# Performance work log

Measured on AMD Instinct MI355X. Metric: run time of the kernel, lower is better.

The kernel has to match this reference:

```python
import jax, jax.numpy as jnp
import numpy as np

B, S, D = 1, 4096, 1024
H, DK, DV = 16, 64, 64


def setup_inputs() -> dict:
    key = jax.random.key(0)
    ks = jax.random.split(key, 12)
    s = 0.02
    return {
        "queries": jax.random.normal(ks[0], (B, S, D), jnp.float32),
        "keys": jax.random.normal(ks[1], (B, S, D), jnp.float32),
        "values": jax.random.normal(ks[2], (B, S, D), jnp.float32),
        "Wq": jax.random.normal(ks[3], (H * DK, D), jnp.float32) * s,
        "bq": jnp.zeros((H * DK,), jnp.float32),
        "Wk": jax.random.normal(ks[4], (H * DK, D), jnp.float32) * s,
        "bk": jnp.zeros((H * DK,), jnp.float32),
        "Wv": jax.random.normal(ks[5], (H * DV, D), jnp.float32) * s,
        "bv": jnp.zeros((H * DV,), jnp.float32),
        "Wo": jax.random.normal(ks[6], (D, H * DV), jnp.float32) * s,
        "bo": jnp.zeros((D,), jnp.float32),
    }


def reference(queries, keys, values, Wq, bq, Wk, bk, Wv, bv, Wo, bo):
    b, sq, _ = queries.shape
    sk = keys.shape[1]
    # projections -> [b, h, s, d]
    q = (queries @ Wq.T + bq).reshape(b, sq, H, DK).transpose(0, 2, 1, 3)
    k = (keys @ Wk.T + bk).reshape(b, sk, H, DK).transpose(0, 2, 1, 3)
    v = (values @ Wv.T + bv).reshape(b, sk, H, DV).transpose(0, 2, 1, 3)
    scores = jnp.einsum('bhqd,bhkd->bhqk', q, k) / jnp.sqrt(jnp.float32(DK))
    # causal mask (is_causal=True): disallow j > i
    causal = jnp.triu(jnp.ones((sq, sk), bool), k=1)
    scores = jnp.where(causal, jnp.float32(-jnp.inf), scores)
    attn = jax.nn.softmax(scores, axis=-1)
    out = jnp.einsum('bhqk,bhkd->bhqd', attn, v)
    out = out.transpose(0, 2, 1, 3).reshape(b, sq, H * DV)
    return out @ Wo.T + bo
```

## Files before the change

### kernel.cpp

```cpp
#include <hip/hip_runtime.h>

#define DEVI __device__ __forceinline__

typedef __attribute__((ext_vector_type(8))) short bf16x8;
typedef __attribute__((ext_vector_type(4))) float f32x4;
typedef __attribute__((ext_vector_type(16))) float f32x16;

#define SQL 4096
#define DM 1024
#define NH 16
#define HD 64
#define S64 (SQL * HD)

DEVI unsigned short f2bf(float f) {
  unsigned int u = __float_as_uint(f);
  unsigned int r = (u + 0x7FFFu + ((u >> 16) & 1u)) >> 16;
  return (unsigned short)r;
}

DEVI void gl16(const void* g, void* l) {
  __builtin_amdgcn_global_load_lds((const __attribute__((address_space(1))) void*)g,
                                   (__attribute__((address_space(3))) void*)l, 16, 0, 0);
}

DEVI f32x4 mfma16(bf16x8 a, bf16x8 b, f32x4 c) {
  return __builtin_amdgcn_mfma_f32_16x16x32_bf16(a, b, c, 0, 0, 0);
}
DEVI f32x16 mfma32(bf16x8 a, bf16x8 b, f32x16 c) {
  return __builtin_amdgcn_mfma_f32_32x32x16_bf16(a, b, c, 0, 0, 0);
}

DEVI unsigned cvtpk(float lo, float hi) {
  unsigned r;
  asm("v_cvt_pk_bf16_f32 %0, %1, %2" : "=v"(r) : "v"(lo), "v"(hi));
  return r;
}

__global__ void cvt_all(const float* __restrict__ q, const float* __restrict__ k,
                        const float* __restrict__ v, const float* __restrict__ Wq,
                        const float* __restrict__ Wk, const float* __restrict__ Wv,
                        const float* __restrict__ Wo, unsigned short* __restrict__ o) {
  const size_t SD = (size_t)SQL * DM, DD = (size_t)DM * DM;
  size_t i = ((size_t)blockIdx.x * 256 + threadIdx.x) * 4;
  const float* src;
  size_t base;
  if (i < SD) { src = q; base = 0; }
  else if (i < 2 * SD) { src = k; base = SD; }
  else if (i < 3 * SD) { src = v; base = 2 * SD; }
  else if (i < 3 * SD + DD) { src = Wq; base = 3 * SD; }
  else if (i < 3 * SD + 2 * DD) { src = Wk; base = 3 * SD + DD; }
  else if (i < 3 * SD + 3 * DD) { src = Wv; base = 3 * SD + 2 * DD; }
  else { src = Wo; base = 3 * SD + 3 * DD; }
  float4 vv = *reinterpret_cast<const float4*>(src + (i - base));
  ushort4 ov;
  ov.x = f2bf(vv.x); ov.y = f2bf(vv.y); ov.z = f2bf(vv.z); ov.w = f2bf(vv.w);
  *reinterpret_cast<ushort4*>(o + i) = ov;
}

__global__ __launch_bounds__(256) void gemm_qkv(
    const unsigned short* __restrict__ xq, const unsigned short* __restrict__ xk,
    const unsigned short* __restrict__ xv, const unsigned short* __restrict__ wq,
    const unsigned short* __restrict__ wk, const unsigned short* __restrict__ wv,
    const float* __restrict__ bq, const float* __restrict__ bk, const float* __restrict__ bv,
    unsigned short* __restrict__ Qh, unsigned short* __restrict__ Kh,
    unsigned short* __restrict__ VT) {
  __shared__ __align__(16) unsigned short smem[17408];
  unsigned short* lA = smem;
  unsigned short* lB = smem + 8192;
  const int z = blockIdx.z;
  const unsigned short* A = (z == 0) ? xq : (z == 1) ? xk : xv;
  const unsigned short* B = (z == 0) ? wq : (z == 1) ? wk : wv;
  const float* bias = (z == 0) ? bq : (z == 1) ? bk : bv;

  const int t = threadIdx.x;
  const int wid = t >> 6, lane = t & 63, lr = lane & 15, lg = lane >> 4;
  const int wm = wid >> 1, wn = wid & 1;
  const int m0 = blockIdx.y * 128, n0 = blockIdx.x * 128;
  const int K = DM;

  f32x4 acc[4][4] = {};

  for (int kb = 0; kb < K; kb += 64) {
    __syncthreads();
#pragma unroll
    for (int i = 0; i < 4; i++) {
      const int u = i * 256 + t;
      const int row = u >> 3;
      const int ke = (u & 7) * 8;
      unsigned short* la = lA + (size_t)(i * 256 + wid * 64) * 8;
      unsigned short* lb = lB + (size_t)(i * 256 + wid * 64) * 8;
      gl16(A + (size_t)(m0 + row) * K + kb + ke, la);
      gl16(B + (size_t)(n0 + row) * K + kb + ke, lb);
    }
    __syncthreads();
#pragma unroll
    for (int kk = 0; kk < 2; kk++) {
      bf16x8 af[4], bfr[4];
#pragma unroll
      for (int m = 0; m < 4; m++)
        af[m] = *reinterpret_cast<const bf16x8*>(&lA[(wm * 64 + m * 16 + lr) * 64 + kk * 32 + lg * 8]);
#pragma unroll
      for (int n = 0; n < 4; n++)
        bfr[n] = *reinterpret_cast<const bf16x8*>(&lB[(wn * 64 + n * 16 + lr) * 64 + kk * 32 + lg * 8]);
#pragma unroll
      for (int m = 0; m < 4; m++)
#pragma unroll
        for (int n = 0; n < 4; n++)
          acc[m][n] = mfma16(af[m], bfr[n], acc[m][n]);
    }
  }

  if (z < 2) {
    const float sc = (z == 0) ? 0.18033688f : 1.0f;
    unsigned short* dst = (z == 0) ? Qh : Kh;
#pragma unroll
    for (int m = 0; m < 4; m++)
#pragma unroll
      for (int n = 0; n < 4; n++) {
        const int col = n0 + wn * 64 + n * 16 + lr;
        const int hh = col >> 6, d = col & 63;
        const int row0 = m0 + wm * 64 + m * 16 + lg * 4;
        const float bsv = bias[col];
#pragma unroll
        for (int r = 0; r < 4; r++)
          dst[(size_t)hh * S64 + (size_t)(row0 + r) * HD + d] = f2bf((acc[m][n][r] + bsv) * sc);
      }
  } else {
    __syncthreads();
#pragma unroll
    for (int m = 0; m < 4; m++)
#pragma unroll
      for (int n = 0; n < 4; n++) {
        const int col = n0 + wn * 64 + n * 16 + lr;
        const int dt = wn * 64 + n * 16 + lr;
        const float bsv = bias[col];
#pragma unroll
        for (int r = 0; r < 4; r++) {
          const int st = wm * 64 + m * 16 + lg * 4 + r;
          smem[dt * 136 + st] = f2bf(acc[m][n][r] + bsv);
        }
      }
    __syncthreads();
#pragma unroll
    for (int it = 0; it < 8; it++) {
      const int u = it * 256 + t;
      const int d = u >> 4, sc8 = (u & 15) * 8;
      const int col = n0 + d, hh = col >> 6, dd = col & 63;
      *reinterpret_cast<uint4*>(VT + (size_t)hh * S64 + (size_t)dd * SQL + m0 + sc8) =
          *reinterpret_cast<const uint4*>(&smem[d * 136 + sc8]);
    }
  }
}

__global__ __launch_bounds__(256) void gemm_out(
    const unsigned short* __restrict__ A, const unsigned short* __restrict__ B,
    const float* __restrict__ bias, float* __restrict__ C) {
  __shared__ __align__(16) unsigned short lA[128 * 64];
  __shared__ __align__(16) unsigned short lB[128 * 64];
  const int t = threadIdx.x;
  const int wid = t >> 6, lane = t & 63, lr = lane & 15, lg = lane >> 4;
  const int wm = wid >> 1, wn = wid & 1;
  const int m0 = blockIdx.y * 128, n0 = blockIdx.x * 128;
  const int K = DM, N = DM;

  f32x4 acc[4][4] = {};

  for (int kb = 0; kb < K; kb += 64) {
    __syncthreads();
#pragma unroll
    for (int i = 0; i < 4; i++) {
      const int u = i * 256 + t;
      const int row = u >> 3;
      const int ke = (u & 7) * 8;
      unsigned short* la = lA + (size_t)(i * 256 + wid * 64) * 8;
      unsigned short* lb = lB + (size_t)(i * 256 + wid * 64) * 8;
      gl16(A + (size_t)(m0 + row) * K + kb + ke, la);
      gl16(B + (size_t)(n0 + row) * K + kb + ke, lb);
    }
    __syncthreads();
#pragma unroll
    for (int kk = 0; kk < 2; kk++) {
      bf16x8 af[4], bfr[4];
#pragma unroll
      for (int m = 0; m < 4; m++)
        af[m] = *reinterpret_cast<const bf16x8*>(&lA[(wm * 64 + m * 16 + lr) * 64 + kk * 32 + lg * 8]);
#pragma unroll
      for (int n = 0; n < 4; n++)
        bfr[n] = *reinterpret_cast<const bf16x8*>(&lB[(wn * 64 + n * 16 + lr) * 64 + kk * 32 + lg * 8]);
#pragma unroll
      for (int m = 0; m < 4; m++)
#pragma unroll
        for (int n = 0; n < 4; n++)
          acc[m][n] = mfma16(af[m], bfr[n], acc[m][n]);
    }
  }

#pragma unroll
  for (int m = 0; m < 4; m++)
#pragma unroll
    for (int n = 0; n < 4; n++)
#pragma unroll
      for (int r = 0; r < 4; r++) {
        const int row = m0 + wm * 64 + m * 16 + lg * 4 + r;
        const int col = n0 + wn * 64 + n * 16 + lr;
        C[(size_t)row * N + col] = acc[m][n][r] + bias[col];
      }
}

__global__ __launch_bounds__(128) void attn_fwd(
    const unsigned short* __restrict__ Qh, const unsigned short* __restrict__ Kh,
    const unsigned short* __restrict__ VT, unsigned short* __restrict__ Ob) {
  const int bid = blockIdx.x;
  const int h = bid & 15;
  const int i6 = bid >> 4;
  const int jj = i6 & 15, bb = i6 >> 4;
  const int qt = (bb & 1) ? (bb * 16 + 15 - jj) : (bb * 16 + jj);
  const int t = threadIdx.x;
  const int wid = t >> 6, lane = t & 63;
  const int ql = lane & 31, hi = lane >> 5;
  const int q0 = qt * 64;
  const int q_g = q0 + wid * 32 + ql;

  __shared__ __align__(16) unsigned short Kt[2][4096];
  __shared__ __align__(16) unsigned short Vt[2][4096];

  const unsigned short* Kp = Kh + (size_t)h * S64;
  const unsigned short* Vp = VT + (size_t)h * S64;

  bf16x8 qf[4];
  {
    const unsigned short* qp = Qh + (size_t)h * S64 + (size_t)q_g * HD + hi * 8;
#pragma unroll
    for (int c = 0; c < 4; c++)
      qf[c] = *reinterpret_cast<const bf16x8*>(qp + c * 16);
  }

  f32x16 accO[2] = {};
  float m = -INFINITY, l = 0.f;

  const int xm = (ql & 7) << 4;
  const int ntile = qt + 1;

#pragma unroll
  for (int ro = 0; ro < 4; ro++) {
    const int u = ro * 128 + t;
    const int row = u >> 3, slot = (u & 7) ^ (row & 7);
    gl16(Kp + (size_t)row * HD + slot * 8, &Kt[0][(ro * 128 + wid * 64) * 8]);
    gl16(Vp + (size_t)row * SQL + slot * 8, &Vt[0][(ro * 128 + wid * 64) * 8]);
  }

  int cur = 0;
  for (int tk = 0; tk < ntile; tk++) {
    const int kv0 = tk * 64;
    __syncthreads();

    if (tk + 1 < ntile) {
      const int nkv = kv0 + 64;
      unsigned short* kdb = Kt[cur ^ 1];
      unsigned short* vdb = Vt[cur ^ 1];
#pragma unroll
      for (int ro = 0; ro < 4; ro++) {
        const int u = ro * 128 + t;
        const int row = u >> 3, slot = (u & 7) ^ (row & 7);
        gl16(Kp + (size_t)(nkv + row) * HD + slot * 8, kdb + (ro * 128 + wid * 64) * 8);
        gl16(Vp + (size_t)row * SQL + nkv + slot * 8, vdb + (ro * 128 + wid * 64) * 8);
      }
    }

    const char* kt = (const char*)Kt[cur];
    const char* vt = (const char*)Vt[cur];

    f32x16 sA[2];
    __builtin_amdgcn_s_setprio(1);
#pragma unroll
    for (int kc = 0; kc < 2; kc++) {
      const char* rb = kt + (32 * kc + ql) * 128;
      f32x16 a = {};
#pragma unroll
      for (int c = 0; c < 4; c++) {
        bf16x8 kf = *reinterpret_cast<const bf16x8*>(rb + ((c * 32 + hi * 16) ^ xm));
        a = mfma32(kf, qf[c], a);
      }
      sA[kc] = a;
    }
    __builtin_amdgcn_s_setprio(0);

    if (tk == qt) {
#pragma unroll
      for (int kc = 0; kc < 2; kc++)
#pragma unroll
        for (int r = 0; r < 16; r++) {
          const int kv_g = kv0 + 32 * kc + (r & 3) + 8 * (r >> 2) + 4 * hi;
          if (kv_g > q_g) sA[kc][r] = -INFINITY;
        }
    }

    float pm = sA[0][0];
#pragma unroll
    for (int r = 1; r < 16; r++) pm = fmaxf(pm, sA[0][r]);
#pragma unroll
    for (int r = 0; r < 16; r++) pm = fmaxf(pm, sA[1][r]);
    pm = fmaxf(pm, __shfl_xor(pm, 32));
    if (!__all(pm - m <= 8.f)) {
      const float mn = fmaxf(m, pm);
      const float al = exp2f(m - mn);
      m = mn;
      l *= al;
#pragma unroll
      for (int dc = 0; dc < 2; dc++)
#pragma unroll
        for (int r = 0; r < 16; r++) accO[dc][r] *= al;
    }
    float sum = 0.f;
#pragma unroll
    for (int kc = 0; kc < 2; kc++)
#pragma unroll
      for (int r = 0; r < 16; r++) {
        const float e = exp2f(sA[kc][r] - m);
        sA[kc][r] = e;
        sum += e;
      }
    sum += __shfl_xor(sum, 32);
    l += sum;

    bf16x8 pf[4];
#pragma unroll
    for (int ck = 0; ck < 4; ck++) {
      const int kc = ck >> 1, rb0 = (ck & 1) * 8;
      unsigned lo0 = cvtpk(sA[kc][rb0 + 0], sA[kc][rb0 + 1]);
      unsigned lo1 = cvtpk(sA[kc][rb0 + 2], sA[kc][rb0 + 3]);
      unsigned h0  = cvtpk(sA[kc][rb0 + 4], sA[kc][rb0 + 5]);
      unsigned h1  = cvtpk(sA[kc][rb0 + 6], sA[kc][rb0 + 7]);
      unsigned xl0 = (unsigned)__shfl_xor((int)lo0, 32);
      unsigned xl1 = (unsigned)__shfl_xor((int)lo1, 32);
      unsigned xh0 = (unsigned)__shfl_xor((int)h0, 32);
      unsigned xh1 = (unsigned)__shfl_xor((int)h1, 32);
      unsigned* pw = (unsigned*)&pf[ck];
      pw[0] = hi ? xh0 : lo0;
      pw[1] = hi ? xh1 : lo1;
      pw[2] = hi ? h0 : xl0;
      pw[3] = hi ? h1 : xl1;
    }

    __builtin_amdgcn_s_setprio(1);
#pragma unroll
    for (int dc = 0; dc < 2; dc++) {
      const char* rb = vt + (32 * dc + ql) * 128;
#pragma unroll
      for (int ck = 0; ck < 4; ck++) {
        bf16x8 vf = *reinterpret_cast<const bf16x8*>(rb + ((ck * 32 + hi * 16) ^ xm));
        accO[dc] = mfma32(vf, pf[ck], accO[dc]);
      }
    }
    __builtin_amdgcn_s_setprio(0);
    cur ^= 1;
  }

  const float inv = 1.f / l;
  unsigned short* ob = Ob + (size_t)q_g * DM + h * HD;
#pragma unroll
  for (int dc = 0; dc < 2; dc++)
#pragma unroll
    for (int tq = 0; tq < 4; tq++) {
      ushort4 o;
      o.x = f2bf(accO[dc][tq * 4 + 0] * inv);
      o.y = f2bf(accO[dc][tq * 4 + 1] * inv);
      o.z = f2bf(accO[dc][tq * 4 + 2] * inv);
      o.w = f2bf(accO[dc][tq * 4 + 3] * inv);
      *reinterpret_cast<ushort4*>(ob + dc * 32 + tq * 8 + hi * 4) = o;
    }
}

extern "C" void kernel_launch(void* const* d_in, const int* in_sizes, int n_in,
                              void* d_out, int out_size, void* d_ws, size_t ws_size,
                              hipStream_t stream) {
  const float* queries = (const float*)d_in[0];
  const float* keys    = (const float*)d_in[1];
  const float* values  = (const float*)d_in[2];
  const float* Wq = (const float*)d_in[3];
  const float* bq = (const float*)d_in[4];
  const float* Wk = (const float*)d_in[5];
  const float* bk = (const float*)d_in[6];
  const float* Wv = (const float*)d_in[7];
  const float* bv = (const float*)d_in[8];
  const float* Wo = (const float*)d_in[9];
  const float* bo = (const float*)d_in[10];
  float* out = (float*)d_out;

  const size_t SD = (size_t)SQL * DM;
  const size_t DD = (size_t)DM * DM;

  unsigned short* p = (unsigned short*)d_ws;
  unsigned short* xq = p; p += SD;
  unsigned short* xk = p; p += SD;
  unsigned short* xv = p; p += SD;
  unsigned short* wq = p; p += DD;
  unsigned short* wk = p; p += DD;
  unsigned short* wv = p; p += DD;
  unsigned short* wo = p; p += DD;
  unsigned short* Qh = p; p += SD;
  unsigned short* Kh = p; p += SD;
  unsigned short* VTg = p; p += SD;
  unsigned short* Ob = xq;

  const int ncvt = (int)((3 * SD + 4 * DD) / 1024);
  cvt_all<<<ncvt, 256, 0, stream>>>(queries, keys, values, Wq, Wk, Wv, Wo, xq);

  gemm_qkv<<<dim3(DM / 128, SQL / 128, 3), 256, 0, stream>>>(
      xq, xk, xv, wq, wk, wv, bq, bk, bv, Qh, Kh, VTg);

  attn_fwd<<<1024, 128, 0, stream>>>(Qh, Kh, VTg, Ob);

  gemm_out<<<dim3(DM / 128, SQL / 128), 256, 0, stream>>>(Ob, wo, bo, out);
}
```

Before: 322.5 us.

## Make attention waves independent with per-wave KV tiles and paired causal load balancing

Each of the two waves in a block now handles its own 32-query tile, paired so one wave takes tile u and the other tile 127-u, which balances causal work inside the block. KV tiles shrink to 32 keys, and each wave stages them through registers into its own padded LDS buffers. This removes __syncthreads and the async global-to-LDS loads. Padding rows to 136/72 bytes replaces the XOR swizzle for avoiding bank conflicts. In exchange there are twice as many loop iterations, each with less MFMA work, plus redundant K/V loads per wave and a register-staged prefetch that costs VGPRs.

```diff
diff --git a/kernel.cpp b/kernel.cpp
--- a/kernel.cpp
+++ b/kernel.cpp
@@ -34,6 +34,13 @@
   unsigned r;
   asm("v_cvt_pk_bf16_f32 %0, %1, %2" : "=v"(r) : "v"(lo), "v"(hi));
   return r;
+}
+
+DEVI bf16x8 ld_b64x2(const char* p) {
+  union { uint2 u[2]; bf16x8 v; } x;
+  x.u[0] = *(const uint2*)p;
+  x.u[1] = *(const uint2*)(p + 8);
+  return x.v;
 }
 
 __global__ void cvt_all(const float* __restrict__ q, const float* __restrict__ k,
@@ -207,22 +214,24 @@
       }
 }
 
+#define KB 32
+#define KROW 136
+#define VROW 72
+#define VOFF (KB * KROW)
+#define BUFSZ (VOFF + HD * VROW)
 __global__ __launch_bounds__(128) void attn_fwd(
     const unsigned short* __restrict__ Qh, const unsigned short* __restrict__ Kh,
     const unsigned short* __restrict__ VT, unsigned short* __restrict__ Ob) {
   const int bid = blockIdx.x;
   const int h = bid & 15;
-  const int i6 = bid >> 4;
-  const int jj = i6 & 15, bb = i6 >> 4;
-  const int qt = (bb & 1) ? (bb * 16 + 15 - jj) : (bb * 16 + jj);
+  const int u6 = bid >> 4;
   const int t = threadIdx.x;
   const int wid = t >> 6, lane = t & 63;
   const int ql = lane & 31, hi = lane >> 5;
-  const int q0 = qt * 64;
-  const int q_g = q0 + wid * 32 + ql;
-
-  __shared__ __align__(16) unsigned short Kt[2][4096];
-  __shared__ __align__(16) unsigned short Vt[2][4096];
+  const int T = wid ? (127 - u6) : u6;
+  const int q_g = T * 32 + ql;
+
+  __shared__ __align__(16) char lds[2][2][BUFSZ];
 
   const unsigned short* Kp = Kh + (size_t)h * S64;
   const unsigned short* Vp = VT + (size_t)h * S64;
@@ -237,69 +246,80 @@
 
   f32x16 accO[2] = {};
   float m = -INFINITY, l = 0.f;
-
-  const int xm = (ql & 7) << 4;
-  const int ntile = qt + 1;
-
-#pragma unroll
-  for (int ro = 0; ro < 4; ro++) {
-    const int u = ro * 128 + t;
-    const int row = u >> 3, slot = (u & 7) ^ (row & 7);
-    gl16(Kp + (size_t)row * HD + slot * 8, &Kt[0][(ro * 128 + wid * 64) * 8]);
-    gl16(Vp + (size_t)row * SQL + slot * 8, &Vt[0][(ro * 128 + wid * 64) * 8]);
+  const int ntile = T + 1;
+
+  uint4 g[8];
+#pragma unroll
+  for (int i = 0; i < 4; i++) {
+    const int v = i * 64 + lane, r = v >> 3, p = v & 7;
+    g[i] = *(const uint4*)(Kp + (size_t)r * HD + p * 8);
+  }
+#pragma unroll
+  for (int i = 0; i < 4; i++) {
+    const int v = i * 64 + lane, r = v >> 2, p = v & 3;
+    g[4 + i] = *(const uint4*)(Vp + (size_t)r * SQL + p * 8);
+  }
+  {
+    char* d0 = &lds[wid][0][0];
+#pragma unroll
+    for (int i = 0; i < 4; i++) {
+      const int v = i * 64 + lane, r = v >> 3, p = v & 7;
+      char* d = d0 + r * KROW + p * 16;
+      *(uint2*)d = make_uint2(g[i].x, g[i].y);
+      *(uint2*)(d + 8) = make_uint2(g[i].z, g[i].w);
+    }
+#pragma unroll
+    for (int i = 0; i < 4; i++) {
+      const int v = i * 64 + lane, r = v >> 2, p = v & 3;
+      char* d = d0 + VOFF + r * VROW + p * 16;
+      *(uint2*)d = make_uint2(g[4 + i].x, g[4 + i].y);
+      *(uint2*)(d + 8) = make_uint2(g[4 + i].z, g[4 + i].w);
+    }
   }
 
   int cur = 0;
   for (int tk = 0; tk < ntile; tk++) {
-    const int kv0 = tk * 64;
-    __syncthreads();
-
-    if (tk + 1 < ntile) {
-      const int nkv = kv0 + 64;
-      unsigned short* kdb = Kt[cur ^ 1];
-      unsigned short* vdb = Vt[cur ^ 1];
-#pragma unroll
-      for (int ro = 0; ro < 4; ro++) {
-        const int u = ro * 128 + t;
-        const int row = u >> 3, slot = (u & 7) ^ (row & 7);
-        gl16(Kp + (size_t)(nkv + row) * HD + slot * 8, kdb + (ro * 128 + wid * 64) * 8);
-        gl16(Vp + (size_t)row * SQL + nkv + slot * 8, vdb + (ro * 128 + wid * 64) * 8);
-      }
-    }
-
-    const char* kt = (const char*)Kt[cur];
-    const char* vt = (const char*)Vt[cur];
-
-    f32x16 sA[2];
+    const int kv0 = tk * KB;
+    const bool pre = (tk + 1 < ntile);
+    if (pre) {
+      const int nkv = kv0 + KB;
+#pragma unroll
+      for (int i = 0; i < 4; i++) {
+        const int v = i * 64 + lane, r = v >> 3, p = v & 7;
+        g[i] = *(const uint4*)(Kp + (size_t)(nkv + r) * HD + p * 8);
+      }
+#pragma unroll
+      for (int i = 0; i < 4; i++) {
+        const int v = i * 64 + lane, r = v >> 2, p = v & 3;
+        g[4 + i] = *(const uint4*)(Vp + (size_t)r * SQL + nkv + p * 8);
+      }
+    }
+
+    const char* kb = &lds[wid][cur][0];
+
+    f32x16 sA = {};
     __builtin_amdgcn_s_setprio(1);
 #pragma unroll
-    for (int kc = 0; kc < 2; kc++) {
-      const char* rb = kt + (32 * kc + ql) * 128;
-      f32x16 a = {};
-#pragma unroll
-      for (int c = 0; c < 4; c++) {
-        bf16x8 kf = *reinterpret_cast<const bf16x8*>(rb + ((c * 32 + hi * 16) ^ xm));
-        a = mfma32(kf, qf[c], a);
-      }
-      sA[kc] = a;
+    for (int c = 0; c < 4; c++) {
+      bf16x8 kf = ld_b64x2(kb + ql * KROW + (2 * c + hi) * 16);
+      sA = mfma32(kf, qf[c], sA);
     }
     __builtin_amdgcn_s_setprio(0);
 
-    if (tk == qt) {
-#pragma unroll
-      for (int kc = 0; kc < 2; kc++)
-#pragma unroll
-        for (int r = 0; r < 16; r++) {
-          const int kv_g = kv0 + 32 * kc + (r & 3) + 8 * (r >> 2) + 4 * hi;
-          if (kv_g > q_g) sA[kc][r] = -INFINITY;
-        }
-    }
-
-    float pm = sA[0][0];
-#pragma unroll
-    for (int r = 1; r < 16; r++) pm = fmaxf(pm, sA[0][r]);
-#pragma unroll
-    for (int r = 0; r < 16; r++) pm = fmaxf(pm, sA[1][r]);
+    if (tk == T) {
+#pragma unroll
+      for (int r = 0; r < 16; r++) {
+        const int kv_g = kv0 + (r & 3) + 8 * (r >> 2) + 4 * hi;
+        if (kv_g > q_g) sA[r] = -INFINITY;
+      }
+    }
+
+    float m0a = fmaxf(sA[0], sA[1]), m1a = fmaxf(sA[2], sA[3]);
+    float m2a = fmaxf(sA[4], sA[5]), m3a = fmaxf(sA[6], sA[7]);
+    float m4a = fmaxf(sA[8], sA[9]), m5a = fmaxf(sA[10], sA[11]);
+    float m6a = fmaxf(sA[12], sA[13]), m7a = fmaxf(sA[14], sA[15]);
+    float pm = fmaxf(fmaxf(fmaxf(m0a, m1a), fmaxf(m2a, m3a)),
+                     fmaxf(fmaxf(m4a, m5a), fmaxf(m6a, m7a)));
     pm = fmaxf(pm, __shfl_xor(pm, 32));
     if (!__all(pm - m <= 8.f)) {
       const float mn = fmaxf(m, pm);
@@ -313,46 +333,60 @@
     }
     float sum = 0.f;
 #pragma unroll
-    for (int kc = 0; kc < 2; kc++)
-#pragma unroll
-      for (int r = 0; r < 16; r++) {
-        const float e = exp2f(sA[kc][r] - m);
-        sA[kc][r] = e;
-        sum += e;
-      }
+    for (int r = 0; r < 16; r++) {
+      const float e = exp2f(sA[r] - m);
+      sA[r] = e;
+      sum += e;
+    }
     sum += __shfl_xor(sum, 32);
     l += sum;
 
-    bf16x8 pf[4];
-#pragma unroll
-    for (int ck = 0; ck < 4; ck++) {
-      const int kc = ck >> 1, rb0 = (ck & 1) * 8;
-      unsigned lo0 = cvtpk(sA[kc][rb0 + 0], sA[kc][rb0 + 1]);
-      unsigned lo1 = cvtpk(sA[kc][rb0 + 2], sA[kc][rb0 + 3]);
-      unsigned h0  = cvtpk(sA[kc][rb0 + 4], sA[kc][rb0 + 5]);
-      unsigned h1  = cvtpk(sA[kc][rb0 + 6], sA[kc][rb0 + 7]);
-      unsigned xl0 = (unsigned)__shfl_xor((int)lo0, 32);
-      unsigned xl1 = (unsigned)__shfl_xor((int)lo1, 32);
-      unsigned xh0 = (unsigned)__shfl_xor((int)h0, 32);
-      unsigned xh1 = (unsigned)__shfl_xor((int)h1, 32);
+    bf16x8 pf[2];
+#pragma unroll
+    for (int ck = 0; ck < 2; ck++) {
+      const int bo = (2 * ck + hi) << 2;
+      const int bs = (2 * ck + (1 - hi)) << 2;
+      unsigned own0 = cvtpk(sA[bo + 0], sA[bo + 1]);
+      unsigned own1 = cvtpk(sA[bo + 2], sA[bo + 3]);
+      unsigned snd0 = cvtpk(sA[bs + 0], sA[bs + 1]);
+      unsigned snd1 = cvtpk(sA[bs + 2], sA[bs + 3]);
+      unsigned rcv0 = (unsigned)__shfl_xor((int)snd0, 32);
+      unsigned rcv1 = (unsigned)__shfl_xor((int)snd1, 32);
       unsigned* pw = (unsigned*)&pf[ck];
-      pw[0] = hi ? xh0 : lo0;
-      pw[1] = hi ? xh1 : lo1;
-      pw[2] = hi ? h0 : xl0;
-      pw[3] = hi ? h1 : xl1;
+      pw[0] = hi ? rcv0 : own0;
+      pw[1] = hi ? rcv1 : own1;
+      pw[2] = hi ? own0 : rcv0;
+      pw[3] = hi ? own1 : rcv1;
     }
 
     __builtin_amdgcn_s_setprio(1);
 #pragma unroll
     for (int dc = 0; dc < 2; dc++) {
-      const char* rb = vt + (32 * dc + ql) * 128;
-#pragma unroll
-      for (int ck = 0; ck < 4; ck++) {
-        bf16x8 vf = *reinterpret_cast<const bf16x8*>(rb + ((ck * 32 + hi * 16) ^ xm));
+#pragma unroll
+      for (int ck = 0; ck < 2; ck++) {
+        bf16x8 vf = ld_b64x2(kb + VOFF + (32 * dc + ql) * VROW + (2 * ck + hi) * 16);
         accO[dc] = mfma32(vf, pf[ck], accO[dc]);
       }
     }
     __builtin_amdgcn_s_setprio(0);
+
+    if (pre) {
+      char* d0 = &lds[wid][cur ^ 1][0];
+#pragma unroll
+      for (int i = 0; i < 4; i++) {
+        const int v = i * 64 + lane, r = v >> 3, p = v & 7;
+        char* d = d0 + r * KROW + p * 16;
+        *(uint2*)d = make_uint2(g[i].x, g[i].y);
+        *(uint2*)(d + 8) = make_uint2(g[i].z, g[i].w);
+      }
+#pragma unroll
+      for (int i = 0; i < 4; i++) {
+        const int v = i * 64 + lane, r = v >> 2, p = v & 3;
+        char* d = d0 + VOFF + r * VROW + p * 16;
+        *(uint2*)d = make_uint2(g[4 + i].x, g[4 + i].y);
+        *(uint2*)(d + 8) = make_uint2(g[4 + i].z, g[4 + i].w);
+      }
+    }
     cur ^= 1;
   }
 
```

Measured after the change: 552.8 us. +71.4%, slower.
